# Kernel tuning notes

Hardware: AMD Instinct MI355X
Metric: run time of the kernel (lower is better)

The kernel has to match this reference:

```python
import jax, jax.numpy as jnp
import numpy as np
import math

N, E, H, A = 50000, 800000, 128, 8
D = H // A


def setup_inputs() -> dict:
    key = jax.random.key(0)
    ks = jax.random.split(key, 12)
    q = jax.random.normal(ks[0], (N, H), dtype=jnp.float32)
    k = jax.random.normal(ks[1], (N, H), dtype=jnp.float32)
    v = jax.random.normal(ks[2], (N, H), dtype=jnp.float32)
    Wq = jax.random.normal(ks[3], (H, H), dtype=jnp.float32) * 0.05
    bq = jax.random.normal(ks[4], (H,), dtype=jnp.float32) * 0.05
    Wk = jax.random.normal(ks[5], (H, H), dtype=jnp.float32) * 0.05
    bk = jax.random.normal(ks[6], (H,), dtype=jnp.float32) * 0.05
    Wv = jax.random.normal(ks[7], (H, H), dtype=jnp.float32) * 0.05
    bv = jax.random.normal(ks[8], (H,), dtype=jnp.float32) * 0.05
    # Ensure every node id appears at least once in q_indices so that
    # q_indices.unique() == arange(N) and the output shape is static [N, H].
    tail = jax.random.randint(ks[9], (E - N,), 0, N)
    q_indices = jnp.concatenate([jnp.arange(N), tail]).astype(jnp.int32)
    k_indices = jax.random.randint(ks[10], (E,), 0, N).astype(jnp.int32)
    return {"q": q, "k": k, "v": v, "Wq": Wq, "bq": bq, "Wk": Wk, "bk": bk,
            "Wv": Wv, "bv": bv, "q_indices": q_indices, "k_indices": k_indices}


def reference(q, k, v, Wq, bq, Wk, bk, Wv, bv, q_indices, k_indices):
    n = q.shape[0]
    # Gather node features per edge (irregular access).
    qe = q[q_indices]            # [E, H]
    ke = k[k_indices]            # [E, H]
    ve = v[k_indices]            # [E, H]
    # Linear projections (torch Linear: x @ W.T + b), split heads -> [E, A, D].
    Q = (qe @ Wq.T + bq).reshape(-1, A, D)
    K = (ke @ Wk.T + bk).reshape(-1, A, D)
    V = (ve @ Wv.T + bv).reshape(-1, A, D)
    # Per-edge scaled dot-product scores: [E, A].
    scores = jnp.einsum('ead,ead->ea', Q, K) / math.sqrt(D)
    # Segment softmax over edges sharing the same destination node
    # (faithful to the original: plain exp, no max subtraction).
    ex = jnp.exp(scores)                                        # [E, A]
    denom = jax.ops.segment_sum(ex, q_indices, num_segments=n)  # [N, A]
    probs = ex / denom[q_indices]                               # [E, A]
    # Scatter-aggregate weighted values per destination node: [N, A, D].
    ctx = jax.ops.segment_sum(probs[:, :, None] * V, q_indices, num_segments=n)
    # Merge heads -> [N, H].
    return ctx.reshape(n, A * D)
```

## Files before the change

### kernel.cpp

```cpp
#include <hip/hip_runtime.h>
#include <hip/hip_bf16.h>

#define HDIM 128
#define LDS_STRIDE 136

typedef __attribute__((ext_vector_type(8))) short bf16x8;
typedef __attribute__((ext_vector_type(4))) float f32x4;

__device__ inline unsigned short f2bf(float f) {
    return __builtin_bit_cast(unsigned short, __float2bfloat16(f));
}
__device__ inline float bflo(unsigned u) { return __uint_as_float(u << 16); }
__device__ inline float bfhi(unsigned u) { return __uint_as_float(u & 0xffff0000u); }

__global__ void init_kernel(int* __restrict__ deg, int n,
                            const float* __restrict__ Wq, const float* __restrict__ Wk,
                            const float* __restrict__ Wv, unsigned short* __restrict__ Wopt) {
    int i = blockIdx.x * 256 + threadIdx.x;
    if (i < n) deg[i] = 0;
    if (i < 3 * HDIM * HDIM) {
        int j  = i & 7;
        int l  = (i >> 3) & 63;
        int ks = (i >> 9) & 3;
        int nt = (i >> 11) & 7;
        int m  = i >> 14;
        const float* W = (m == 0) ? Wq : (m == 1) ? Wk : Wv;
        int row = nt * 16 + (l & 15);
        int col = ks * 32 + ((l >> 4) << 3) + j;
        Wopt[i] = f2bf(W[row * HDIM + col]);
    }
}

__global__ void proj_deg(const float* __restrict__ qin, const float* __restrict__ kin,
                         const float* __restrict__ vin, const unsigned short* __restrict__ Wopt,
                         const float* __restrict__ bq, const float* __restrict__ bk,
                         const float* __restrict__ bv,
                         unsigned short* __restrict__ Qb, unsigned short* __restrict__ Kb,
                         unsigned short* __restrict__ Vb,
                         const int* __restrict__ qidx, int* __restrict__ deg,
                         int* __restrict__ rank, int E, int n, int nbx, int ndeg, int ntot)
{
    __shared__ unsigned short tile[64 * LDS_STRIDE];

    const int id     = blockIdx.x;
    const int before = (int)(((long)id * ndeg) / ntot);
    const bool isdeg = (int)(((long)(id + 1) * ndeg) / ntot) > before;

    if (isdeg) {
        const int e0 = before * 1024 + (int)threadIdx.x * 4;
        if (e0 + 4 <= E) {
            const int4 qi = *(const int4*)&qidx[e0];
            int4 r;
            r.x = atomicAdd(&deg[qi.x], 1);
            r.y = atomicAdd(&deg[qi.y], 1);
            r.z = atomicAdd(&deg[qi.z], 1);
            r.w = atomicAdd(&deg[qi.w], 1);
            *(int4*)&rank[e0] = r;
        } else {
            #pragma unroll
            for (int j = 0; j < 4; ++j)
                if (e0 + j < E) rank[e0 + j] = atomicAdd(&deg[qidx[e0 + j]], 1);
        }
        return;
    }

    const int pid = id - before;
    const int m   = pid / nbx;
    const int bx  = pid - m * nbx;

    const int tid  = threadIdx.x;
    const int lane = tid & 63;
    const int wv   = tid >> 6;
    const long node0 = (long)bx * 64;

    const float* x = (m == 0) ? qin : (m == 1) ? kin : vin;
    const float* b = (m == 0) ? bq  : (m == 1) ? bk  : bv;
    unsigned short* O = (m == 0) ? Qb : (m == 1) ? Kb : Vb;
    const unsigned short* Wm = Wopt + (size_t)m * HDIM * HDIM;

    #pragma unroll
    for (int it = 0; it < 8; ++it) {
        int f   = it * 256 + tid;
        int row = f >> 5;
        int c4  = f & 31;
        long node = node0 + row;
        float4 val = make_float4(0.f, 0.f, 0.f, 0.f);
        if (node < n) val = ((const float4*)(x + node * HDIM))[c4];
        ushort4 h;
        h.x = f2bf(val.x); h.y = f2bf(val.y); h.z = f2bf(val.z); h.w = f2bf(val.w);
        *(ushort4*)&tile[row * LDS_STRIDE + c4 * 4] = h;
    }
    __syncthreads();

    const int r15  = lane & 15;
    const int quad = lane >> 4;

    bf16x8 af[4];
    #pragma unroll
    for (int ks = 0; ks < 4; ++ks)
        af[ks] = *(const bf16x8*)&tile[(wv * 16 + r15) * LDS_STRIDE + quad * 8 + ks * 32];

    f32x4 acc[8];
    #pragma unroll
    for (int nt = 0; nt < 8; ++nt) {
        acc[nt] = (f32x4){0.f, 0.f, 0.f, 0.f};
        #pragma unroll
        for (int ks = 0; ks < 4; ++ks) {
            const bf16x8 wfrag =
                *(const bf16x8*)(Wm + ((size_t)((nt * 4 + ks) * 64) + lane) * 8);
            acc[nt] = __builtin_amdgcn_mfma_f32_16x16x32_bf16(af[ks], wfrag, acc[nt], 0, 0, 0);
        }
    }
    __syncthreads();

    #pragma unroll
    for (int nt = 0; nt < 8; ++nt) {
        const int c = nt * 16 + r15;
        const float bias = b[c];
        #pragma unroll
        for (int r = 0; r < 4; ++r)
            tile[(wv * 16 + quad * 4 + r) * LDS_STRIDE + c] = f2bf(acc[nt][r] + bias);
    }
    __syncthreads();

    #pragma unroll
    for (int it = 0; it < 4; ++it) {
        int g   = it * 256 + tid;
        int row = g >> 4;
        int col = (g & 15) * 8;
        long node = node0 + row;
        if (node < n) {
            ushort4 lo = *(const ushort4*)&tile[row * LDS_STRIDE + col];
            ushort4 hi = *(const ushort4*)&tile[row * LDS_STRIDE + col + 4];
            uint4 out4;
            out4.x = (unsigned)lo.x | ((unsigned)lo.y << 16);
            out4.y = (unsigned)lo.z | ((unsigned)lo.w << 16);
            out4.z = (unsigned)hi.x | ((unsigned)hi.y << 16);
            out4.w = (unsigned)hi.z | ((unsigned)hi.w << 16);
            *(uint4*)&O[node * HDIM + col] = out4;
        }
    }
}

__global__ void scan_block(const int* __restrict__ deg, int* __restrict__ offs,
                           int* __restrict__ bsum, int n) {
    __shared__ int ws[17];
    const int tid = threadIdx.x;
    const int lane = tid & 63, wv = tid >> 6;
    int i = blockIdx.x * 1024 + tid;
    int v = (i < n) ? deg[i] : 0;
    int sc = v;
    #pragma unroll
    for (int d = 1; d < 64; d <<= 1) {
        int t = __shfl_up(sc, d, 64);
        if (lane >= d) sc += t;
    }
    if (lane == 63) ws[wv] = sc;
    __syncthreads();
    if (tid == 0) {
        int base = 0;
        #pragma unroll
        for (int w = 0; w < 16; ++w) { int t = ws[w]; ws[w] = base; base += t; }
        ws[16] = base;
    }
    __syncthreads();
    if (i < n) offs[i] = ws[wv] + (sc - v);
    if (tid == 0) bsum[blockIdx.x] = ws[16];
}

__global__ void scan_addtops(const int* __restrict__ bsum, int* __restrict__ offs,
                             int n, int E, int nb) {
    __shared__ int s_base;
    const int tid = threadIdx.x;
    if (tid < 64) {
        int v = (tid < nb) ? bsum[tid] : 0;
        int sc = v;
        #pragma unroll
        for (int d = 1; d < 64; d <<= 1) {
            int t = __shfl_up(sc, d, 64);
            if (tid >= d) sc += t;
        }
        if (tid == blockIdx.x) s_base = sc - v;
    }
    __syncthreads();
    int i = blockIdx.x * 1024 + tid;
    if (i < n) offs[i] += s_base;
    if (blockIdx.x == 0 && tid == 0) offs[n] = E;
}

__global__ void fill_kernel(const int* __restrict__ qidx, const int* __restrict__ kidx,
                            const int* __restrict__ offs, const int* __restrict__ rank,
                            int* __restrict__ srcl, int E) {
    int e0 = (blockIdx.x * 256 + (int)threadIdx.x) * 4;
    if (e0 + 4 <= E) {
        const int4 qi = *(const int4*)&qidx[e0];
        const int4 ki = *(const int4*)&kidx[e0];
        const int4 rk = *(const int4*)&rank[e0];
        srcl[offs[qi.x] + rk.x] = ki.x;
        srcl[offs[qi.y] + rk.y] = ki.y;
        srcl[offs[qi.z] + rk.z] = ki.z;
        srcl[offs[qi.w] + rk.w] = ki.w;
    } else {
        #pragma unroll
        for (int j = 0; j < 4; ++j)
            if (e0 + j < E) srcl[offs[qidx[e0 + j]] + rank[e0 + j]] = kidx[e0 + j];
    }
}

__global__ void agg_kernel(const uint2* __restrict__ Q2, const uint2* __restrict__ K2,
                           const uint2* __restrict__ V2,
                           const int* __restrict__ offs, const int* __restrict__ srcl,
                           float* __restrict__ out, int n)
{
    const int tid  = threadIdx.x;
    const int l32  = tid & 31;
    const int node = blockIdx.x * 8 + (tid >> 5);
    if (node >= n) return;

    const uint2 qp = Q2[(size_t)node * 32 + l32];
    const float qx = bflo(qp.x), qy = bfhi(qp.x), qz = bflo(qp.y), qw = bfhi(qp.y);

    float dsum = 0.f, a0 = 0.f, a1 = 0.f, a2 = 0.f, a3 = 0.f;
    const int beg = offs[node], end = offs[node + 1];
    const int srcbase = tid & 32;

#define EDGE_STEP(kp, vp)                                                      \
    {                                                                          \
        float part = qx * bflo((kp).x) + qy * bfhi((kp).x)                     \
                   + qz * bflo((kp).y) + qw * bfhi((kp).y);                    \
        part += __shfl_xor(part, 1, 64);                                       \
        part += __shfl_xor(part, 2, 64);                                       \
        float w = __expf(part * 0.25f);                                        \
        dsum += w;                                                             \
        a0 += w * bflo((vp).x); a1 += w * bfhi((vp).x);                        \
        a2 += w * bflo((vp).y); a3 += w * bfhi((vp).y);                        \
    }

    for (int base = beg; base < end; base += 32) {
        int cnt = min(32, end - base);
        int my = (base + l32 < end) ? srcl[base + l32] : 0;
        int j = 0;
        for (; j + 2 <= cnt; j += 2) {
            int s0 = __shfl(my, srcbase + j,     64);
            int s1 = __shfl(my, srcbase + j + 1, 64);
            uint2 k0 = K2[(size_t)s0 * 32 + l32];
            uint2 v0 = V2[(size_t)s0 * 32 + l32];
            uint2 k1 = K2[(size_t)s1 * 32 + l32];
            uint2 v1 = V2[(size_t)s1 * 32 + l32];
            EDGE_STEP(k0, v0); EDGE_STEP(k1, v1);
        }
        for (; j < cnt; ++j) {
            int s = __shfl(my, srcbase + j, 64);
            uint2 kk = K2[(size_t)s * 32 + l32];
            uint2 vv = V2[(size_t)s * 32 + l32];
            EDGE_STEP(kk, vv);
        }
    }
#undef EDGE_STEP

    float inv = 1.f / dsum;
    float4 r = make_float4(a0 * inv, a1 * inv, a2 * inv, a3 * inv);
    *(float4*)&out[(size_t)node * HDIM + l32 * 4] = r;
}

extern "C" void kernel_launch(void* const* d_in, const int* in_sizes, int n_in,
                              void* d_out, int out_size, void* d_ws, size_t ws_size,
                              hipStream_t stream) {
    const float* q  = (const float*)d_in[0];
    const float* k  = (const float*)d_in[1];
    const float* v  = (const float*)d_in[2];
    const float* Wq = (const float*)d_in[3];
    const float* bq = (const float*)d_in[4];
    const float* Wk = (const float*)d_in[5];
    const float* bk = (const float*)d_in[6];
    const float* Wv = (const float*)d_in[7];
    const float* bv = (const float*)d_in[8];
    const int* qidx = (const int*)d_in[9];
    const int* kidx = (const int*)d_in[10];
    float* out = (float*)d_out;

    const int N = in_sizes[0] / HDIM;
    const int E = in_sizes[9];

    char* p = (char*)d_ws;
    unsigned short* Qb = (unsigned short*)p; p += (size_t)N * HDIM * sizeof(unsigned short);
    unsigned short* Kb = (unsigned short*)p; p += (size_t)N * HDIM * sizeof(unsigned short);
    unsigned short* Vb = (unsigned short*)p; p += (size_t)N * HDIM * sizeof(unsigned short);
    unsigned short* Wopt = (unsigned short*)p; p += (size_t)3 * HDIM * HDIM * sizeof(unsigned short);
    int* deg  = (int*)p; p += (size_t)N * sizeof(int);
    int* offs = (int*)p; p += (size_t)(N + 1) * sizeof(int);
    int* bsum = (int*)p; p += 64 * sizeof(int);
    int* rank = (int*)p; p += (size_t)E * sizeof(int);
    int* srcl = (int*)p; p += (size_t)E * sizeof(int);

    const int nbx  = (N + 63) / 64;
    const int ndeg = (E + 1023) / 1024;
    const int ntot = 3 * nbx + ndeg;
    const int nfb  = (E + 1023) / 1024;
    const int nb   = (N + 1023) / 1024;
    const int initn = (N > 3 * HDIM * HDIM) ? N : 3 * HDIM * HDIM;

    init_kernel<<<(initn + 255) / 256, 256, 0, stream>>>(deg, N, Wq, Wk, Wv, Wopt);
    proj_deg<<<ntot, 256, 0, stream>>>(q, k, v, Wopt, bq, bk, bv, Qb, Kb, Vb,
                                       qidx, deg, rank, E, N, nbx, ndeg, ntot);
    scan_block<<<nb, 1024, 0, stream>>>(deg, offs, bsum, N);
    scan_addtops<<<nb, 1024, 0, stream>>>(bsum, offs, N, E, nb);
    fill_kernel<<<nfb, 256, 0, stream>>>(qidx, kidx, offs, rank, srcl, E);
    agg_kernel<<<(N + 7) / 8, 256, 0, stream>>>((const uint2*)Qb, (const uint2*)Kb,
                                                (const uint2*)Vb, offs, srcl, out, N);
}
```

Before: 233.9 us.

## Interleave K and V projections into one buffer for single gather per edge

The projection kernel now writes K and V into one interleaved buffer, so each node's row holds, per 4-element group, the K values followed by the matching V values. The aggregation kernel then loads one 16-byte uint4 per lane per edge instead of two separate 8-byte loads from distinct K and V arrays. The edge loop is also unrolled from 2 to 4 edges per iteration to keep more gathers in flight. This is meant to halve the number of irregular memory transactions per edge and improve row locality. The cost is strided 8-byte stores in the projection and more register pressure in the aggregation loop.

```diff
diff --git a/kernel.cpp b/kernel.cpp
--- a/kernel.cpp
+++ b/kernel.cpp
@@ -35,8 +35,7 @@
                          const float* __restrict__ vin, const unsigned short* __restrict__ Wopt,
                          const float* __restrict__ bq, const float* __restrict__ bk,
                          const float* __restrict__ bv,
-                         unsigned short* __restrict__ Qb, unsigned short* __restrict__ Kb,
-                         unsigned short* __restrict__ Vb,
+                         unsigned short* __restrict__ Qb, unsigned short* __restrict__ KVb,
                          const int* __restrict__ qidx, int* __restrict__ deg,
                          int* __restrict__ rank, int E, int n, int nbx, int ndeg, int ntot)
 {
@@ -75,7 +74,6 @@
 
     const float* x = (m == 0) ? qin : (m == 1) ? kin : vin;
     const float* b = (m == 0) ? bq  : (m == 1) ? bk  : bv;
-    unsigned short* O = (m == 0) ? Qb : (m == 1) ? Kb : Vb;
     const unsigned short* Wm = Wopt + (size_t)m * HDIM * HDIM;
 
     #pragma unroll
@@ -132,12 +130,19 @@
         if (node < n) {
             ushort4 lo = *(const ushort4*)&tile[row * LDS_STRIDE + col];
             ushort4 hi = *(const ushort4*)&tile[row * LDS_STRIDE + col + 4];
-            uint4 out4;
-            out4.x = (unsigned)lo.x | ((unsigned)lo.y << 16);
-            out4.y = (unsigned)lo.z | ((unsigned)lo.w << 16);
-            out4.z = (unsigned)hi.x | ((unsigned)hi.y << 16);
-            out4.w = (unsigned)hi.z | ((unsigned)hi.w << 16);
-            *(uint4*)&O[node * HDIM + col] = out4;
+            uint2 plo, phi;
+            plo.x = (unsigned)lo.x | ((unsigned)lo.y << 16);
+            plo.y = (unsigned)lo.z | ((unsigned)lo.w << 16);
+            phi.x = (unsigned)hi.x | ((unsigned)hi.y << 16);
+            phi.y = (unsigned)hi.z | ((unsigned)hi.w << 16);
+            if (m == 0) {
+                uint4 out4; out4.x = plo.x; out4.y = plo.y; out4.z = phi.x; out4.w = phi.y;
+                *(uint4*)&Qb[node * HDIM + col] = out4;
+            } else {
+                size_t base = (size_t)node * 256 + (size_t)col * 2 + ((m == 2) ? 4 : 0);
+                *(uint2*)&KVb[base]     = plo;
+                *(uint2*)&KVb[base + 8] = phi;
+            }
         }
     }
 }
@@ -207,8 +212,7 @@
     }
 }
 
-__global__ void agg_kernel(const uint2* __restrict__ Q2, const uint2* __restrict__ K2,
-                           const uint2* __restrict__ V2,
+__global__ void agg_kernel(const uint2* __restrict__ Q2, const uint4* __restrict__ KV4,
                            const int* __restrict__ offs, const int* __restrict__ srcl,
                            float* __restrict__ out, int n)
 {
@@ -224,36 +228,37 @@
     const int beg = offs[node], end = offs[node + 1];
     const int srcbase = tid & 32;
 
-#define EDGE_STEP(kp, vp)                                                      \
+#define EDGE_STEP(kv)                                                          \
     {                                                                          \
-        float part = qx * bflo((kp).x) + qy * bfhi((kp).x)                     \
-                   + qz * bflo((kp).y) + qw * bfhi((kp).y);                    \
+        float part = qx * bflo((kv).x) + qy * bfhi((kv).x)                     \
+                   + qz * bflo((kv).y) + qw * bfhi((kv).y);                    \
         part += __shfl_xor(part, 1, 64);                                       \
         part += __shfl_xor(part, 2, 64);                                       \
         float w = __expf(part * 0.25f);                                        \
         dsum += w;                                                             \
-        a0 += w * bflo((vp).x); a1 += w * bfhi((vp).x);                        \
-        a2 += w * bflo((vp).y); a3 += w * bfhi((vp).y);                        \
+        a0 += w * bflo((kv).z); a1 += w * bfhi((kv).z);                        \
+        a2 += w * bflo((kv).w); a3 += w * bfhi((kv).w);                        \
     }
 
     for (int base = beg; base < end; base += 32) {
         int cnt = min(32, end - base);
         int my = (base + l32 < end) ? srcl[base + l32] : 0;
         int j = 0;
-        for (; j + 2 <= cnt; j += 2) {
+        for (; j + 4 <= cnt; j += 4) {
             int s0 = __shfl(my, srcbase + j,     64);
             int s1 = __shfl(my, srcbase + j + 1, 64);
-            uint2 k0 = K2[(size_t)s0 * 32 + l32];
-            uint2 v0 = V2[(size_t)s0 * 32 + l32];
-            uint2 k1 = K2[(size_t)s1 * 32 + l32];
-            uint2 v1 = V2[(size_t)s1 * 32 + l32];
-            EDGE_STEP(k0, v0); EDGE_STEP(k1, v1);
+            int s2 = __shfl(my, srcbase + j + 2, 64);
+            int s3 = __shfl(my, srcbase + j + 3, 64);
+            uint4 kv0 = KV4[(size_t)s0 * 32 + l32];
+            uint4 kv1 = KV4[(size_t)s1 * 32 + l32];
+            uint4 kv2 = KV4[(size_t)s2 * 32 + l32];
+            uint4 kv3 = KV4[(size_t)s3 * 32 + l32];
+            EDGE_STEP(kv0); EDGE_STEP(kv1); EDGE_STEP(kv2); EDGE_STEP(kv3);
         }
         for (; j < cnt; ++j) {
             int s = __shfl(my, srcbase + j, 64);
-            uint2 kk = K2[(size_t)s * 32 + l32];
-            uint2 vv = V2[(size_t)s * 32 + l32];
-            EDGE_STEP(kk, vv);
+            uint4 kv = KV4[(size_t)s * 32 + l32];
+            EDGE_STEP(kv);
         }
     }
 #undef EDGE_STEP
@@ -283,9 +288,8 @@
     const int E = in_sizes[9];
 
     char* p = (char*)d_ws;
-    unsigned short* Qb = (unsigned short*)p; p += (size_t)N * HDIM * sizeof(unsigned short);
-    unsigned short* Kb = (unsigned short*)p; p += (size_t)N * HDIM * sizeof(unsigned short);
-    unsigned short* Vb = (unsigned short*)p; p += (size_t)N * HDIM * sizeof(unsigned short);
+    unsigned short* Qb  = (unsigned short*)p; p += (size_t)N * HDIM * sizeof(unsigned short);
+    unsigned short* KVb = (unsigned short*)p; p += (size_t)2 * N * HDIM * sizeof(unsigned short);
     unsigned short* Wopt = (unsigned short*)p; p += (size_t)3 * HDIM * HDIM * sizeof(unsigned short);
     int* deg  = (int*)p; p += (size_t)N * sizeof(int);
     int* offs = (int*)p; p += (size_t)(N + 1) * sizeof(int);
@@ -301,11 +305,11 @@
     const int initn = (N > 3 * HDIM * HDIM) ? N : 3 * HDIM * HDIM;
 
     init_kernel<<<(initn + 255) / 256, 256, 0, stream>>>(deg, N, Wq, Wk, Wv, Wopt);
-    proj_deg<<<ntot, 256, 0, stream>>>(q, k, v, Wopt, bq, bk, bv, Qb, Kb, Vb,
+    proj_deg<<<ntot, 256, 0, stream>>>(q, k, v, Wopt, bq, bk, bv, Qb, KVb,
                                        qidx, deg, rank, E, N, nbx, ndeg, ntot);
     scan_block<<<nb, 1024, 0, stream>>>(deg, offs, bsum, N);
     scan_addtops<<<nb, 1024, 0, stream>>>(bsum, offs, N, E, nb);
     fill_kernel<<<nfb, 256, 0, stream>>>(qidx, kidx, offs, rank, srcl, E);
-    agg_kernel<<<(N + 7) / 8, 256, 0, stream>>>((const uint2*)Qb, (const uint2*)Kb,
-                                                (const uint2*)Vb, offs, srcl, out, N);
-}
+    agg_kernel<<<(N + 7) / 8, 256, 0, stream>>>((const uint2*)Qb, (const uint4*)KVb,
+                                                offs, srcl, out, N);
+}
```

Result: slower. 245.6 us (+5.0%).
